# Optimization experiments

Measured on AMD Instinct MI355X. Metric: run time of the kernel, lower is better.

## Reference

```python
import jax, jax.numpy as jnp
import numpy as np

WIN = 8
SHIFT = WIN // 2  # shift=True
NH = 12
HD = 32
EPS = 1e-5


def _rel_pos_index(w):
    coords = np.stack(np.meshgrid(np.arange(w), np.arange(w), indexing='ij')).reshape(2, -1)
    rel = (coords[:, :, None] - coords[:, None, :]).transpose(1, 2, 0)
    rel[..., 0] += w - 1
    rel[..., 1] += w - 1
    rel[..., 0] *= 2 * w - 1
    return rel.sum(-1)  # [w*w, w*w]

REL_IDX = jnp.asarray(_rel_pos_index(WIN), dtype=jnp.int32)


def _ln(x, g, b):
    mu = jnp.mean(x, axis=-1, keepdims=True)
    var = jnp.mean(jnp.square(x - mu), axis=-1, keepdims=True)
    return (x - mu) * jax.lax.rsqrt(var + EPS) * g + b


def setup_inputs() -> dict:
    key = jax.random.key(0)
    ks = jax.random.split(key, 8)
    B, Hh, Ww, C = 16, 64, 64, 384
    s = lambda fan: 1.0 / np.sqrt(fan)
    return {
        'x': jax.random.normal(ks[0], (B, Hh * Ww, C), jnp.float32),
        'norm1_g': jnp.ones((C,), jnp.float32),
        'norm1_b': jnp.zeros((C,), jnp.float32),
        'qkv_w': jax.random.normal(ks[1], (3 * C, C), jnp.float32) * s(C),
        'qkv_b': jnp.zeros((3 * C,), jnp.float32),
        'proj_w': jax.random.normal(ks[2], (C, C), jnp.float32) * s(C),
        'proj_b': jnp.zeros((C,), jnp.float32),
        'rpb_table': jax.random.normal(ks[3], ((2 * WIN - 1) ** 2, NH), jnp.float32) * 0.02,
        'norm2_g': jnp.ones((C,), jnp.float32),
        'norm2_b': jnp.zeros((C,), jnp.float32),
        'fc1_w': jax.random.normal(ks[4], (4 * C, C), jnp.float32) * s(C),
        'fc1_b': jnp.zeros((4 * C,), jnp.float32),
        'fc2_w': jax.random.normal(ks[5], (C, 4 * C), jnp.float32) * s(4 * C),
        'fc2_b': jnp.zeros((C,), jnp.float32),
        'H': Hh,
        'W': Ww,
    }


def reference(x, norm1_g, norm1_b, qkv_w, qkv_b, proj_w, proj_b, rpb_table,
              norm2_g, norm2_b, fc1_w, fc1_b, fc2_w, fc2_b, H, W):
    B, N, C = x.shape
    Nw = WIN * WIN
    shortcut = x
    h = _ln(x, norm1_g, norm1_b)

    # window partition with roll (shifted windows)
    h = h.reshape(B, H, W, C)
    h = jnp.roll(h, shift=(-SHIFT, -SHIFT), axis=(1, 2))
    h = h.reshape(B, H // WIN, WIN, W // WIN, WIN, C).transpose(0, 1, 3, 2, 4, 5)
    h = h.reshape(-1, Nw, C)  # [B*nW, 64, C]

    # window attention
    qkv = h @ qkv_w.T + qkv_b  # [Bw, Nw, 3C]
    qkv = qkv.reshape(-1, Nw, 3, NH, HD).transpose(2, 0, 3, 1, 4)
    q, k, v = qkv[0], qkv[1], qkv[2]  # [Bw, NH, Nw, HD]
    attn = jnp.einsum('bhqd,bhkd->bhqk', q, k) * (HD ** -0.5)
    bias = rpb_table[REL_IDX.reshape(-1)].reshape(Nw, Nw, NH).transpose(2, 0, 1)
    attn = jax.nn.softmax(attn + bias[None], axis=-1)
    o = jnp.einsum('bhqk,bhkd->bhqd', attn, v)
    o = o.transpose(0, 2, 1, 3).reshape(-1, Nw, C)
    o = o @ proj_w.T + proj_b

    # window reverse with inverse roll
    o = o.reshape(B, H // WIN, W // WIN, WIN, WIN, C).transpose(0, 1, 3, 2, 4, 5)
    o = o.reshape(B, H, W, C)
    o = jnp.roll(o, shift=(SHIFT, SHIFT), axis=(1, 2)).reshape(B, N, C)

    x = shortcut + o
    m = _ln(x, norm2_g, norm2_b)
    m = jax.nn.gelu(m @ fc1_w.T + fc1_b, approximate=False)
    m = m @ fc2_w.T + fc2_b
    return x + m
```

## Files before the change

### kernel.cpp

```cpp
#include <hip/hip_runtime.h>
#include <hip/hip_bf16.h>
#include <math.h>

typedef __attribute__((ext_vector_type(8))) short bf16x8;
typedef __attribute__((ext_vector_type(4))) float f32x4;
typedef unsigned short u16;

#define NHEAD 12
#define MATS 25165824
#define HEADS 2097152

__device__ __forceinline__ u16 f2bf(float f) {
  __hip_bfloat16 h = __float2bfloat16(f);
  return __builtin_bit_cast(u16, h);
}

__device__ __forceinline__ void gload16(const void* g, void* l) {
  __builtin_amdgcn_global_load_lds(
      (const __attribute__((address_space(1))) void*)g,
      (__attribute__((address_space(3))) void*)l, 16, 0, 0);
}

__global__ void cvt_all(const float* __restrict__ s0, const float* __restrict__ s1,
                        const float* __restrict__ s2, const float* __restrict__ s3,
                        u16* __restrict__ d) {
  int i = blockIdx.x * 256 + threadIdx.x;
  if (i >= 1769472) return;
  float v;
  if (i < 442368) v = s0[i];
  else if (i < 589824) v = s1[i - 442368];
  else if (i < 1179648) v = s2[i - 589824];
  else v = s3[i - 1179648];
  d[i] = f2bf(v);
}

__global__ void build_bias(const float* __restrict__ rpb, float* __restrict__ bt) {
  int i = blockIdx.x * 256 + threadIdx.x;
  if (i >= NHEAD * 4096) return;
  int h = i >> 12;
  int q = (i >> 6) & 63;
  int k = i & 63;
  int qi = q >> 3, qj = q & 7, ki = k >> 3, kj = k & 7;
  int idx = (qi - ki + 7) * 15 + (qj - kj + 7);
  bt[i] = rpb[idx * NHEAD + h];
}

__global__ __launch_bounds__(256) void ln_k(const float* __restrict__ x,
                                            const float* __restrict__ g,
                                            const float* __restrict__ b,
                                            u16* __restrict__ out) {
  int row = (blockIdx.x << 2) + (threadIdx.x >> 6);
  int lane = threadIdx.x & 63;
  const float* xr = x + (size_t)row * 384;
  float v[6];
  float s = 0.f;
#pragma unroll
  for (int i = 0; i < 6; ++i) { v[i] = xr[lane + (i << 6)]; s += v[i]; }
#pragma unroll
  for (int o = 32; o; o >>= 1) s += __shfl_xor(s, o, 64);
  float mu = s * (1.f / 384.f);
  float vs = 0.f;
#pragma unroll
  for (int i = 0; i < 6; ++i) { float d0 = v[i] - mu; vs += d0 * d0; }
#pragma unroll
  for (int o = 32; o; o >>= 1) vs += __shfl_xor(vs, o, 64);
  float rs = rsqrtf(vs * (1.f / 384.f) + 1e-5f);
  u16* orow = out + (size_t)row * 384;
#pragma unroll
  for (int i = 0; i < 6; ++i) {
    int c = lane + (i << 6);
    orow[c] = f2bf((v[i] - mu) * rs * g[c] + b[c]);
  }
}

template <int EP>
__global__ __launch_bounds__(256, 4) void gemmA(const u16* __restrict__ A,
                                                const u16* __restrict__ W,
                                                const float* __restrict__ bias,
                                                const float* __restrict__ res,
                                                void* __restrict__ outp,
                                                int N, int K, int nCol) {
  __shared__ u16 As[128 * 64];
  __shared__ u16 Bs[128 * 64];
  const int tid = threadIdx.x;
  const int wave = tid >> 6, lane = tid & 63;
  const int wm = wave >> 1, wn = wave & 1;
  const int nwg = gridDim.x, cpx = nwg >> 3;
  const int lin = (blockIdx.x & 7) * cpx + (blockIdx.x >> 3);
  const int rowT = lin / nCol;
  const int colT = lin - rowT * nCol;
  const int rowBase = rowT << 7;
  const int colBase = colT << 7;
  const int nK = K >> 6;

  const int g16 = (tid & 7) ^ ((tid >> 3) & 7);
  const u16* Asrc = A + (size_t)(rowBase + (tid >> 3)) * K + (g16 << 3);
  const u16* Wsrc = W + (size_t)(colBase + (tid >> 3)) * K + (g16 << 3);
  const int ldst = tid << 3;

  const int q4 = lane >> 4;
  const int rx = lane & 7;
  const int arow = (wm << 6) + (lane & 15);
  const int brow = (wn << 6) + (lane & 15);

  f32x4 acc[4][4] = {};

  for (int j = 0; j < nK; ++j) {
    const size_t k0 = (size_t)j << 6;
#pragma unroll
    for (int c = 0; c < 4; ++c) {
      gload16(Asrc + (size_t)(c << 5) * K + k0, &As[(c << 11) + ldst]);
      gload16(Wsrc + (size_t)(c << 5) * K + k0, &Bs[(c << 11) + ldst]);
    }
    __syncthreads();
#pragma unroll
    for (int kk = 0; kk < 2; ++kk) {
      const int slot = (((kk << 2) + q4) ^ rx) << 3;
      bf16x8 aF[4], bF[4];
#pragma unroll
      for (int m = 0; m < 4; ++m)
        aF[m] = *(const bf16x8*)&As[(arow + (m << 4)) * 64 + slot];
#pragma unroll
      for (int n = 0; n < 4; ++n)
        bF[n] = *(const bf16x8*)&Bs[(brow + (n << 4)) * 64 + slot];
#pragma unroll
      for (int m = 0; m < 4; ++m)
#pragma unroll
        for (int n = 0; n < 4; ++n)
          acc[m][n] = __builtin_amdgcn_mfma_f32_16x16x32_bf16(aF[m], bF[n], acc[m][n], 0, 0, 0);
    }
    __syncthreads();
  }

  float bv[4];
#pragma unroll
  for (int n = 0; n < 4; ++n) bv[n] = bias[colBase + (wn << 6) + (n << 4) + (lane & 15)];

  if (EP == 0) {
    int cp[4];
#pragma unroll
    for (int n = 0; n < 4; ++n) {
      int col = colBase + (wn << 6) + (n << 4) + (lane & 15);
      int mat = (col >= 768) ? 2 : (col >= 384 ? 1 : 0);
      int c = col - mat * 384;
      cp[n] = mat * MATS + (c >> 5) * HEADS + (c & 31);
    }
#pragma unroll
    for (int m = 0; m < 4; ++m)
#pragma unroll
      for (int jj = 0; jj < 4; ++jj) {
        int row = rowBase + (wm << 6) + (m << 4) + ((lane >> 4) << 2) + jj;
        int b = row >> 12, R = (row >> 6) & 63, C = row & 63;
        int rt = (R + 60) & 63, ct = (C + 60) & 63;
        int rowpart = (((b << 6) + ((rt >> 3) << 3) + (ct >> 3)) << 11) +
                      ((((rt & 7) << 3) + (ct & 7)) << 5);
#pragma unroll
        for (int n = 0; n < 4; ++n)
          ((u16*)outp)[cp[n] + rowpart] = f2bf(acc[m][n][jj] + bv[n]);
      }
  } else {
#pragma unroll
    for (int m = 0; m < 4; ++m) {
#pragma unroll
      for (int n = 0; n < 4; ++n) {
        const int col = colBase + (wn << 6) + (n << 4) + (lane & 15);
        const int row0 = rowBase + (wm << 6) + (m << 4) + ((lane >> 4) << 2);
#pragma unroll
        for (int jj = 0; jj < 4; ++jj) {
          const size_t row = (size_t)(row0 + jj);
          float y = acc[m][n][jj] + bv[n];
          if (EP == 2) {
            float y2 = y * y;
            float t = __builtin_fmaf(y2, 0.1029434f, 2.3022118f);
            float e = __builtin_amdgcn_exp2f(-(y * t));
            y = y * __builtin_amdgcn_rcpf(1.f + e);
            ((u16*)outp)[row * N + col] = f2bf(y);
          } else {
            ((float*)outp)[row * N + col] = y + res[row * N + col];
          }
        }
      }
    }
  }
}

__global__ __launch_bounds__(512, 4) void projln_k(const u16* __restrict__ A,
                                                   const u16* __restrict__ W,
                                                   const float* __restrict__ bias,
                                                   const float* __restrict__ res,
                                                   const float* __restrict__ g2,
                                                   const float* __restrict__ b2,
                                                   float* __restrict__ x1,
                                                   u16* __restrict__ h2) {
  __shared__ u16 As[64 * 64];
  __shared__ u16 Ws[384 * 64];
  __shared__ float red[2][2][4][32];
  const int tid = threadIdx.x;
  const int wave = tid >> 6, lane = tid & 63;
  const int wm = wave >> 2, wn = wave & 3;
  const int rowBase = blockIdx.x << 6;

  const int g16 = (tid & 7) ^ ((tid >> 3) & 7);
  const u16* Asrc = A + (size_t)(rowBase + (tid >> 3)) * 384 + (g16 << 3);
  const u16* Wsrc = W + (size_t)(tid >> 3) * 384 + (g16 << 3);
  const int ldst = tid << 3;
  const int q4 = lane >> 4, rx = lane & 7;
  const int arow = (wm << 5) + (lane & 15);
  const int brow = wn * 96 + (lane & 15);

  f32x4 acc[2][6] = {};

  for (int j = 0; j < 6; ++j) {
    const size_t k0 = (size_t)j << 6;
    gload16(Asrc + k0, &As[ldst]);
#pragma unroll
    for (int c = 0; c < 6; ++c)
      gload16(Wsrc + (size_t)(c << 6) * 384 + k0, &Ws[(c << 12) + ldst]);
    __syncthreads();
#pragma unroll
    for (int kk = 0; kk < 2; ++kk) {
      const int slot = (((kk << 2) + q4) ^ rx) << 3;
      bf16x8 aF[2], bF[6];
#pragma unroll
      for (int m = 0; m < 2; ++m)
        aF[m] = *(const bf16x8*)&As[(arow + (m << 4)) * 64 + slot];
#pragma unroll
      for (int n = 0; n < 6; ++n)
        bF[n] = *(const bf16x8*)&Ws[(brow + (n << 4)) * 64 + slot];
#pragma unroll
      for (int m = 0; m < 2; ++m)
#pragma unroll
        for (int n = 0; n < 6; ++n)
          acc[m][n] = __builtin_amdgcn_mfma_f32_16x16x32_bf16(aF[m], bF[n], acc[m][n], 0, 0, 0);
    }
    __syncthreads();
  }

  float bv[6], gv[6], b2v[6];
#pragma unroll
  for (int n = 0; n < 6; ++n) {
    int col = wn * 96 + (n << 4) + (lane & 15);
    bv[n] = bias[col]; gv[n] = g2[col]; b2v[n] = b2[col];
  }
#pragma unroll
  for (int m = 0; m < 2; ++m) {
#pragma unroll
    for (int jj = 0; jj < 4; ++jj) {
      int row = rowBase + (wm << 5) + (m << 4) + ((lane >> 4) << 2) + jj;
      const float* rr = res + (size_t)row * 384 + wn * 96 + (lane & 15);
      float s = 0.f, sq = 0.f;
#pragma unroll
      for (int n = 0; n < 6; ++n) {
        float v = acc[m][n][jj] + bv[n] + rr[n << 4];
        acc[m][n][jj] = v;
        s += v; sq += v * v;
      }
#pragma unroll
      for (int o2 = 1; o2 < 16; o2 <<= 1) {
        s += __shfl_xor(s, o2, 64);
        sq += __shfl_xor(sq, o2, 64);
      }
      if ((lane & 15) == 0) {
        int rloc = (m << 4) + ((lane >> 4) << 2) + jj;
        red[0][wm][wn][rloc] = s;
        red[1][wm][wn][rloc] = sq;
      }
    }
  }
  __syncthreads();
#pragma unroll
  for (int m = 0; m < 2; ++m) {
#pragma unroll
    for (int jj = 0; jj < 4; ++jj) {
      int rloc = (m << 4) + ((lane >> 4) << 2) + jj;
      float s = red[0][wm][0][rloc] + red[0][wm][1][rloc] + red[0][wm][2][rloc] + red[0][wm][3][rloc];
      float sq = red[1][wm][0][rloc] + red[1][wm][1][rloc] + red[1][wm][2][rloc] + red[1][wm][3][rloc];
      float mu = s * (1.f / 384.f);
      float var = sq * (1.f / 384.f) - mu * mu;
      float rs = rsqrtf(var + 1e-5f);
      int row = rowBase + (wm << 5) + (m << 4) + ((lane >> 4) << 2) + jj;
      float* xr = x1 + (size_t)row * 384;
      u16* hr = h2 + (size_t)row * 384;
      int cb = wn * 96 + (lane & 15);
#pragma unroll
      for (int n = 0; n < 6; ++n) {
        float v = acc[m][n][jj];
        xr[cb + (n << 4)] = v;
        hr[cb + (n << 4)] = f2bf((v - mu) * rs * gv[n] + b2v[n]);
      }
    }
  }
}

__global__ __launch_bounds__(256) void attn_k(const u16* __restrict__ qkvp,
                                              const float* __restrict__ bias_tab,
                                              u16* __restrict__ o) {
  const int cpx = gridDim.x >> 3;
  const int lin = (blockIdx.x & 7) * cpx + (blockIdx.x >> 3);
  const int w = lin / NHEAD;
  const int h = lin - w * NHEAD;
  const int tid = threadIdx.x, wave = tid >> 6, lane = tid & 63;
  __shared__ u16 q_s[64 * 32];
  __shared__ u16 k_s[64 * 32];
  __shared__ u16 vt_s[32 * 64];
  __shared__ u16 p_s[4][16 * 72];
  const u16* qb = qkvp + (size_t)h * HEADS + (w << 11);
  gload16(qb + tid * 8, &q_s[tid * 8]);
  gload16(qb + MATS + tid * 8, &k_s[tid * 8]);
  {
    const int p = tid >> 2, d0 = (tid & 3) << 3;
    u16 vv[8];
    *(uint4*)vv = *(const uint4*)(qb + 2 * MATS + p * 32 + d0);
#pragma unroll
    for (int jj = 0; jj < 8; ++jj) vt_s[(d0 + jj) * 64 + p] = vv[jj];
  }
  asm volatile("s_waitcnt vmcnt(0)" ::: "memory");
  __syncthreads();
  const int cIdx = lane & 15, rgrp = lane >> 4;
  const f32x4 zz = {0.f, 0.f, 0.f, 0.f};
  bf16x8 qa = *(const bf16x8*)&q_s[((wave << 4) + cIdx) * 32 + (rgrp << 3)];
  f32x4 s_acc[4];
#pragma unroll
  for (int n = 0; n < 4; ++n) {
    bf16x8 kb = *(const bf16x8*)&k_s[((n << 4) + cIdx) * 32 + (rgrp << 3)];
    s_acc[n] = __builtin_amdgcn_mfma_f32_16x16x32_bf16(qa, kb, zz, 0, 0, 0);
  }
  const float scale = 0.1767766952966369f;
  float mrow[4] = {-1e30f, -1e30f, -1e30f, -1e30f};
  const float* bt = bias_tab + h * 4096 + ((wave << 4) + (rgrp << 2)) * 64 + cIdx;
#pragma unroll
  for (int n = 0; n < 4; ++n)
#pragma unroll
    for (int j = 0; j < 4; ++j) {
      float val = s_acc[n][j] * scale + bt[j * 64 + (n << 4)];
      s_acc[n][j] = val;
      mrow[j] = fmaxf(mrow[j], val);
    }
#pragma unroll
  for (int j = 0; j < 4; ++j)
#pragma unroll
    for (int o2 = 1; o2 < 16; o2 <<= 1) mrow[j] = fmaxf(mrow[j], __shfl_xor(mrow[j], o2, 64));
  float srow[4] = {0.f, 0.f, 0.f, 0.f};
#pragma unroll
  for (int n = 0; n < 4; ++n)
#pragma unroll
    for (int j = 0; j < 4; ++j) {
      float e = __expf(s_acc[n][j] - mrow[j]);
      s_acc[n][j] = e;
      srow[j] += e;
    }
#pragma unroll
  for (int j = 0; j < 4; ++j)
#pragma unroll
    for (int o2 = 1; o2 < 16; o2 <<= 1) srow[j] += __shfl_xor(srow[j], o2, 64);
  float rinv[4];
#pragma unroll
  for (int j = 0; j < 4; ++j) rinv[j] = 1.f / srow[j];
  u16* pw = p_s[wave];
#pragma unroll
  for (int n = 0; n < 4; ++n)
#pragma unroll
    for (int j = 0; j < 4; ++j)
      pw[((rgrp << 2) + j) * 72 + (n << 4) + cIdx] = f2bf(s_acc[n][j] * rinv[j]);
  f32x4 o_acc[2] = {};
#pragma unroll
  for (int kk = 0; kk < 2; ++kk) {
    bf16x8 pa = *(const bf16x8*)&pw[cIdx * 72 + (kk << 5) + (rgrp << 3)];
#pragma unroll
    for (int c2 = 0; c2 < 2; ++c2) {
      bf16x8 vb = *(const bf16x8*)&vt_s[((c2 << 4) + cIdx) * 64 + (kk << 5) + (rgrp << 3)];
      o_acc[c2] = __builtin_amdgcn_mfma_f32_16x16x32_bf16(pa, vb, o_acc[c2], 0, 0, 0);
    }
  }
  const int b = w >> 6;
  const int wim = w & 63;
  const int wr0 = (wim >> 3) << 3, wc0 = (wim & 7) << 3;
#pragma unroll
  for (int c2 = 0; c2 < 2; ++c2)
#pragma unroll
    for (int j = 0; j < 4; ++j) {
      const int p = (wave << 4) + (rgrp << 2) + j;
      const int pr = p >> 3, pc = p & 7;
      const int orow = (wr0 + pr + 4) & 63, ocol = (wc0 + pc + 4) & 63;
      const size_t t = ((size_t)b << 12) + (orow << 6) + ocol;
      o[t * 384 + h * 32 + (c2 << 4) + cIdx] = f2bf(o_acc[c2][j]);
    }
}

extern "C" void kernel_launch(void* const* d_in, const int* in_sizes, int n_in,
                              void* d_out, int out_size, void* d_ws, size_t ws_size,
                              hipStream_t stream) {
  const float* x = (const float*)d_in[0];
  const float* n1g = (const float*)d_in[1];
  const float* n1b = (const float*)d_in[2];
  const float* qkv_w = (const float*)d_in[3];
  const float* qkv_b = (const float*)d_in[4];
  const float* proj_w = (const float*)d_in[5];
  const float* proj_b = (const float*)d_in[6];
  const float* rpb = (const float*)d_in[7];
  const float* n2g = (const float*)d_in[8];
  const float* n2b = (const float*)d_in[9];
  const float* fc1_w = (const float*)d_in[10];
  const float* fc1_b = (const float*)d_in[11];
  const float* fc2_w = (const float*)d_in[12];
  const float* fc2_b = (const float*)d_in[13];

  char* ws = (char*)d_ws;
  u16* wqkv = (u16*)(ws + 0);
  u16* wproj = (u16*)(ws + 884736);
  u16* wfc1 = (u16*)(ws + 1179648);
  u16* wfc2 = (u16*)(ws + 2359296);
  float* bias_tab = (float*)(ws + 3538944);
  u16* qkvp = (u16*)(ws + 3735552);
  u16* m1 = qkvp;
  u16* hbuf = (u16*)(ws + 205062144);
  u16* obuf = hbuf;
  float* x1 = (float*)d_out;

  cvt_all<<<(1769472 + 255) / 256, 256, 0, stream>>>(qkv_w, proj_w, fc1_w, fc2_w, wqkv);
  build_bias<<<192, 256, 0, stream>>>(rpb, bias_tab);

  ln_k<<<16384, 256, 0, stream>>>(x, n1g, n1b, hbuf);
  gemmA<0><<<4608, 256, 0, stream>>>(hbuf, wqkv, qkv_b, nullptr, qkvp, 1152, 384, 9);
  attn_k<<<12288, 256, 0, stream>>>(qkvp, bias_tab, obuf);
  projln_k<<<1024, 512, 0, stream>>>(obuf, wproj, proj_b, x, n2g, n2b, x1, hbuf);
  gemmA<2><<<6144, 256, 0, stream>>>(hbuf, wfc1, fc1_b, nullptr, m1, 1536, 384, 12);
  gemmA<3><<<1536, 256, 0, stream>>>(m1, wfc2, fc2_b, x1, (float*)d_out, 384, 1536, 3);
}
```

Baseline: 492.0 us.

## Replace GEMM with 256x192-tile double-buffered 8-wave pipelined kernel

Replaces the 128x128 single-buffered GEMM with a 256x192 tile kernel using 8 waves and double-buffered LDS. Global-to-LDS loads for the next K step are interleaved with MFMA phases, using barriers and raised wave priority around the MFMA blocks. The larger tile is meant to improve data reuse per block, and the split-phase prefetch is meant to hide load latency behind compute. In exchange it uses much more LDS (112 KB) and accumulator registers, which limits occupancy to about one block per CU. The fc2 launch now has only 512 blocks, which may underfill the GPU.

```diff
diff --git a/kernel.cpp b/kernel.cpp
--- a/kernel.cpp
+++ b/kernel.cpp
@@ -74,23 +74,23 @@
 }
 
 template <int EP>
-__global__ __launch_bounds__(256, 4) void gemmA(const u16* __restrict__ A,
+__global__ __launch_bounds__(512, 1) void gemmB(const u16* __restrict__ A,
                                                 const u16* __restrict__ W,
                                                 const float* __restrict__ bias,
                                                 const float* __restrict__ res,
                                                 void* __restrict__ outp,
                                                 int N, int K, int nCol) {
-  __shared__ u16 As[128 * 64];
-  __shared__ u16 Bs[128 * 64];
+  __shared__ u16 As[2][256 * 64];
+  __shared__ u16 Bs[2][192 * 64];
   const int tid = threadIdx.x;
   const int wave = tid >> 6, lane = tid & 63;
-  const int wm = wave >> 1, wn = wave & 1;
+  const int wm = wave >> 2, wn = wave & 3;
   const int nwg = gridDim.x, cpx = nwg >> 3;
   const int lin = (blockIdx.x & 7) * cpx + (blockIdx.x >> 3);
   const int rowT = lin / nCol;
   const int colT = lin - rowT * nCol;
-  const int rowBase = rowT << 7;
-  const int colBase = colT << 7;
+  const int rowBase = rowT << 8;
+  const int colBase = colT * 192;
   const int nK = K >> 6;
 
   const int g16 = (tid & 7) ^ ((tid >> 3) & 7);
@@ -98,81 +98,111 @@
   const u16* Wsrc = W + (size_t)(colBase + (tid >> 3)) * K + (g16 << 3);
   const int ldst = tid << 3;
 
-  const int q4 = lane >> 4;
-  const int rx = lane & 7;
-  const int arow = (wm << 6) + (lane & 15);
-  const int brow = (wn << 6) + (lane & 15);
-
-  f32x4 acc[4][4] = {};
-
-  for (int j = 0; j < nK; ++j) {
-    const size_t k0 = (size_t)j << 6;
-#pragma unroll
-    for (int c = 0; c < 4; ++c) {
-      gload16(Asrc + (size_t)(c << 5) * K + k0, &As[(c << 11) + ldst]);
-      gload16(Wsrc + (size_t)(c << 5) * K + k0, &Bs[(c << 11) + ldst]);
-    }
-    __syncthreads();
-#pragma unroll
-    for (int kk = 0; kk < 2; ++kk) {
-      const int slot = (((kk << 2) + q4) ^ rx) << 3;
-      bf16x8 aF[4], bF[4];
-#pragma unroll
-      for (int m = 0; m < 4; ++m)
-        aF[m] = *(const bf16x8*)&As[(arow + (m << 4)) * 64 + slot];
-#pragma unroll
-      for (int n = 0; n < 4; ++n)
-        bF[n] = *(const bf16x8*)&Bs[(brow + (n << 4)) * 64 + slot];
-#pragma unroll
-      for (int m = 0; m < 4; ++m)
-#pragma unroll
-        for (int n = 0; n < 4; ++n)
-          acc[m][n] = __builtin_amdgcn_mfma_f32_16x16x32_bf16(aF[m], bF[n], acc[m][n], 0, 0, 0);
-    }
-    __syncthreads();
-  }
-
-  float bv[4];
-#pragma unroll
-  for (int n = 0; n < 4; ++n) bv[n] = bias[colBase + (wn << 6) + (n << 4) + (lane & 15)];
+  const int q4 = lane >> 4, rx = lane & 7;
+  const int arow = (wm << 7) + (lane & 15);
+  const int brow = wn * 48 + (lane & 15);
+
+  f32x4 acc[8][3] = {};
+  bf16x8 bF[3];
+
+#pragma unroll
+  for (int r = 0; r < 4; ++r)
+    gload16(Asrc + (size_t)(r << 6) * K, &As[0][(r << 12) + ldst]);
+#pragma unroll
+  for (int r = 0; r < 3; ++r)
+    gload16(Wsrc + (size_t)(r << 6) * K, &Bs[0][(r << 12) + ldst]);
+  asm volatile("s_waitcnt vmcnt(0)" ::: "memory");
+  __builtin_amdgcn_s_barrier();
+
+#define PHASEB(MH, KK, STG, GATE)                                                \
+  {                                                                              \
+    const int slot = ((((KK) << 2) + q4) ^ rx) << 3;                             \
+    bf16x8 aF[4];                                                                \
+    _Pragma("unroll") for (int i = 0; i < 4; ++i)                                \
+        aF[i] = *(const bf16x8*)&ab[(arow + ((((MH) << 2) | i) << 4)) * 64 + slot]; \
+    if ((MH) == 0) {                                                             \
+      _Pragma("unroll") for (int n = 0; n < 3; ++n)                              \
+          bF[n] = *(const bf16x8*)&bb[(brow + (n << 4)) * 64 + slot];            \
+    }                                                                            \
+    STG;                                                                         \
+    __builtin_amdgcn_s_barrier();                                                \
+    asm volatile("s_waitcnt lgkmcnt(0)" ::: "memory");                           \
+    __builtin_amdgcn_sched_barrier(0);                                           \
+    __builtin_amdgcn_s_setprio(1);                                               \
+    _Pragma("unroll") for (int i = 0; i < 4; ++i)                                \
+        _Pragma("unroll") for (int n = 0; n < 3; ++n)                            \
+            acc[(MH)*4 + i][n] = __builtin_amdgcn_mfma_f32_16x16x32_bf16(        \
+                aF[i], bF[n], acc[(MH)*4 + i][n], 0, 0, 0);                      \
+    __builtin_amdgcn_s_setprio(0);                                               \
+    __builtin_amdgcn_sched_barrier(0);                                           \
+    GATE;                                                                        \
+    __builtin_amdgcn_s_barrier();                                                \
+  }
+
+  for (int t = 0; t < nK; ++t) {
+    const int bsel = t & 1;
+    const u16* ab = As[bsel];
+    const u16* bb = Bs[bsel];
+    u16* an = As[bsel ^ 1];
+    u16* bn = Bs[bsel ^ 1];
+    const size_t k1 = (size_t)(t + 1) << 6;
+    const bool pf = (t + 1 < nK);
+    PHASEB(0, 0,
+           if (pf) { gload16(Asrc + k1, &an[ldst]);
+                     gload16(Asrc + (size_t)64 * K + k1, &an[4096 + ldst]); }, )
+    PHASEB(1, 0,
+           if (pf) { gload16(Asrc + (size_t)128 * K + k1, &an[8192 + ldst]);
+                     gload16(Asrc + (size_t)192 * K + k1, &an[12288 + ldst]); }, )
+    PHASEB(0, 1,
+           if (pf) { gload16(Wsrc + k1, &bn[ldst]);
+                     gload16(Wsrc + (size_t)64 * K + k1, &bn[4096 + ldst]); }, )
+    PHASEB(1, 1,
+           if (pf) { gload16(Wsrc + (size_t)128 * K + k1, &bn[8192 + ldst]); },
+           if (pf) { asm volatile("s_waitcnt vmcnt(0)" ::: "memory"); })
+  }
+#undef PHASEB
+
+  float bv[3];
+#pragma unroll
+  for (int n = 0; n < 3; ++n) bv[n] = bias[colBase + wn * 48 + (n << 4) + (lane & 15)];
 
   if (EP == 0) {
-    int cp[4];
-#pragma unroll
-    for (int n = 0; n < 4; ++n) {
-      int col = colBase + (wn << 6) + (n << 4) + (lane & 15);
+    int cp[3];
+#pragma unroll
+    for (int n = 0; n < 3; ++n) {
+      int col = colBase + wn * 48 + (n << 4) + (lane & 15);
       int mat = (col >= 768) ? 2 : (col >= 384 ? 1 : 0);
       int c = col - mat * 384;
       cp[n] = mat * MATS + (c >> 5) * HEADS + (c & 31);
     }
 #pragma unroll
-    for (int m = 0; m < 4; ++m)
+    for (int m = 0; m < 8; ++m)
 #pragma unroll
       for (int jj = 0; jj < 4; ++jj) {
-        int row = rowBase + (wm << 6) + (m << 4) + ((lane >> 4) << 2) + jj;
-        int b = row >> 12, R = (row >> 6) & 63, C = row & 63;
+        int row = rowBase + (wm << 7) + (m << 4) + ((lane >> 4) << 2) + jj;
+        int bb2 = row >> 12, R = (row >> 6) & 63, C = row & 63;
         int rt = (R + 60) & 63, ct = (C + 60) & 63;
-        int rowpart = (((b << 6) + ((rt >> 3) << 3) + (ct >> 3)) << 11) +
+        int rowpart = (((bb2 << 6) + ((rt >> 3) << 3) + (ct >> 3)) << 11) +
                       ((((rt & 7) << 3) + (ct & 7)) << 5);
 #pragma unroll
-        for (int n = 0; n < 4; ++n)
+        for (int n = 0; n < 3; ++n)
           ((u16*)outp)[cp[n] + rowpart] = f2bf(acc[m][n][jj] + bv[n]);
       }
   } else {
 #pragma unroll
-    for (int m = 0; m < 4; ++m) {
-#pragma unroll
-      for (int n = 0; n < 4; ++n) {
-        const int col = colBase + (wn << 6) + (n << 4) + (lane & 15);
-        const int row0 = rowBase + (wm << 6) + (m << 4) + ((lane >> 4) << 2);
+    for (int m = 0; m < 8; ++m) {
+#pragma unroll
+      for (int n = 0; n < 3; ++n) {
+        const int col = colBase + wn * 48 + (n << 4) + (lane & 15);
+        const int row0 = rowBase + (wm << 7) + (m << 4) + ((lane >> 4) << 2);
 #pragma unroll
         for (int jj = 0; jj < 4; ++jj) {
           const size_t row = (size_t)(row0 + jj);
           float y = acc[m][n][jj] + bv[n];
           if (EP == 2) {
             float y2 = y * y;
-            float t = __builtin_fmaf(y2, 0.1029434f, 2.3022118f);
-            float e = __builtin_amdgcn_exp2f(-(y * t));
+            float tt = __builtin_fmaf(y2, 0.1029434f, 2.3022118f);
+            float e = __builtin_amdgcn_exp2f(-(y * tt));
             y = y * __builtin_amdgcn_rcpf(1.f + e);
             ((u16*)outp)[row * N + col] = f2bf(y);
           } else {
@@ -421,9 +451,9 @@
   build_bias<<<192, 256, 0, stream>>>(rpb, bias_tab);
 
   ln_k<<<16384, 256, 0, stream>>>(x, n1g, n1b, hbuf);
-  gemmA<0><<<4608, 256, 0, stream>>>(hbuf, wqkv, qkv_b, nullptr, qkvp, 1152, 384, 9);
+  gemmB<0><<<1536, 512, 0, stream>>>(hbuf, wqkv, qkv_b, nullptr, qkvp, 1152, 384, 6);
   attn_k<<<12288, 256, 0, stream>>>(qkvp, bias_tab, obuf);
   projln_k<<<1024, 512, 0, stream>>>(obuf, wproj, proj_b, x, n2g, n2b, x1, hbuf);
-  gemmA<2><<<6144, 256, 0, stream>>>(hbuf, wfc1, fc1_b, nullptr, m1, 1536, 384, 12);
-  gemmA<3><<<1536, 256, 0, stream>>>(m1, wfc2, fc2_b, x1, (float*)d_out, 384, 1536, 3);
-}
+  gemmB<2><<<2048, 512, 0, stream>>>(hbuf, wfc1, fc1_b, nullptr, m1, 1536, 384, 8);
+  gemmB<3><<<512, 512, 0, stream>>>(m1, wfc2, fc2_b, x1, (float*)d_out, 384, 1536, 2);
+}
```

Result: slower. 550.3 us (+11.9%).
